# Optimization experiments

Hardware: AMD Instinct MI355X
Metric: run time of the kernel (lower is better)

Reference implementation:

```python
import jax, jax.numpy as jnp
import numpy as np

DIM = 2048
H = 16
D = 128          # head_dim
INNER = H * D    # == DIM
N_IMG = 257
EPS = 1e-6


def rms_norm(x, scale, eps=EPS):
    # flax nnx.RMSNorm over last axis: x * rsqrt(mean(x^2)+eps) * scale
    ms = jnp.mean(jnp.square(x), axis=-1, keepdims=True)
    return x * jax.lax.rsqrt(ms + eps) * scale


def sdpa(q, k, v):
    # q: (B,S,H,D), k/v: (B,L,H,D) -> (B,S,H,D); matches jax.nn.dot_product_attention
    scale = 1.0 / jnp.sqrt(jnp.asarray(D, q.dtype))
    scores = jnp.einsum('bshd,blhd->bhsl', q, k) * scale
    attn = jax.nn.softmax(scores, axis=-1)
    return jnp.einsum('bhsl,blhd->bshd', attn, v)


def setup_inputs() -> dict:
    key = jax.random.key(0)
    ks = jax.random.split(key, 16)
    std = 1.0 / np.sqrt(DIM)
    inp = {
        'x': jax.random.normal(ks[0], (2, 4096, DIM), jnp.float32),
        'context': jax.random.normal(ks[1], (2, 769, DIM), jnp.float32),
        'q_w': jax.random.normal(ks[2], (DIM, INNER), jnp.float32) * std,
        'q_b': jnp.zeros((INNER,), jnp.float32),
        'k_w': jax.random.normal(ks[3], (DIM, INNER), jnp.float32) * std,
        'k_b': jnp.zeros((INNER,), jnp.float32),
        'v_w': jax.random.normal(ks[4], (DIM, INNER), jnp.float32) * std,
        'v_b': jnp.zeros((INNER,), jnp.float32),
        'ki_w': jax.random.normal(ks[5], (DIM, INNER), jnp.float32) * std,
        'ki_b': jnp.zeros((INNER,), jnp.float32),
        'vi_w': jax.random.normal(ks[6], (DIM, INNER), jnp.float32) * std,
        'vi_b': jnp.zeros((INNER,), jnp.float32),
        'o_w': jax.random.normal(ks[7], (INNER, DIM), jnp.float32) * std,
        'o_b': jnp.zeros((DIM,), jnp.float32),
        'nq_s': jnp.ones((INNER,), jnp.float32),
        'nkt_s': jnp.ones((INNER,), jnp.float32),
        'nki_s': jnp.ones((INNER,), jnp.float32),
    }
    return inp


def reference(x, context, q_w, q_b, k_w, k_b, v_w, v_b, ki_w, ki_b, vi_w, vi_b,
              o_w, o_b, nq_s, nkt_s, nki_s):
    B, S, _ = x.shape
    img_ctx = context[:, :N_IMG]
    txt_ctx = context[:, N_IMG:]

    q = rms_norm(x @ q_w + q_b, nq_s).reshape(B, S, H, D)

    k_txt = rms_norm(txt_ctx @ k_w + k_b, nkt_s).reshape(B, -1, H, D)
    v_txt = (txt_ctx @ v_w + v_b).reshape(B, -1, H, D)
    out_txt = sdpa(q, k_txt, v_txt)

    k_img = rms_norm(img_ctx @ ki_w + ki_b, nki_s).reshape(B, -1, H, D)
    v_img = (img_ctx @ vi_w + vi_b).reshape(B, -1, H, D)
    out_img = sdpa(q, k_img, v_img)

    out = (out_txt + out_img).reshape(B, S, INNER)
    return out @ o_w + o_b
```

## Files before the change

kernel.cpp:

```cpp
#include <hip/hip_runtime.h>

typedef unsigned short u16;
typedef short s8v __attribute__((ext_vector_type(8)));
typedef float f32x4 __attribute__((ext_vector_type(4)));

#define MFMA16(a, b, c) __builtin_amdgcn_mfma_f32_16x16x32_bf16((a), (b), (c), 0, 0, 0)
#define GLDS16(gp, lp)                                                         \
  __builtin_amdgcn_global_load_lds(                                            \
      (const __attribute__((address_space(1))) void*)(gp),                     \
      (__attribute__((address_space(3))) void*)(lp), 16, 0, 0)

__device__ __forceinline__ float bf2f(u16 u) {
  unsigned int i = ((unsigned int)u) << 16;
  float f;
  __builtin_memcpy(&f, &i, 4);
  return f;
}
__device__ __forceinline__ u16 f2bf(float f) {
  unsigned int u;
  __builtin_memcpy(&u, &f, 4);
  unsigned int r = (u + 0x7FFFu + ((u >> 16) & 1u)) >> 16;
  return (u16)r;
}

__global__ __launch_bounds__(256) void cvt_f32_bf16(const float* __restrict__ s,
                                                    u16* __restrict__ d, long n) {
  long i = ((long)blockIdx.x * 256 + threadIdx.x) * 4;
  if (i + 3 < n) {
    float4 v = *(const float4*)(s + i);
    ushort4 o;
    o.x = f2bf(v.x); o.y = f2bf(v.y); o.z = f2bf(v.z); o.w = f2bf(v.w);
    *(ushort4*)(d + i) = o;
  }
}

struct TransposeBatch {
  const float* src[6];
  u16* dst[6];
};

__global__ __launch_bounds__(256) void transpose2048_batch(TransposeBatch p) {
  const float* __restrict__ W = p.src[blockIdx.z];
  u16* __restrict__ Wt = p.dst[blockIdx.z];
  __shared__ u16 t[64][65];
  int c0 = blockIdx.x * 64, r0 = blockIdx.y * 64;
  int x = threadIdx.x & 63, y = threadIdx.x >> 6;
  for (int yy = y; yy < 64; yy += 4)
    t[yy][x] = f2bf(W[(long)(r0 + yy) * 2048 + c0 + x]);
  __syncthreads();
  for (int yy = y; yy < 64; yy += 4)
    Wt[(long)(c0 + yy) * 2048 + r0 + x] = t[x][yy];
}

template <int OUTF, int DUAL>
__global__ __launch_bounds__(256, 2) void gemm_bias_bt(
    const u16* __restrict__ A, const u16* __restrict__ Bt,
    const float* __restrict__ bias, const float* __restrict__ bias2,
    void* __restrict__ Yv, void* __restrict__ Yv2, int M, int rpb, int bstride,
    int roff) {
  __shared__ u16 smA[128 * 32];
  __shared__ u16 smB[128 * 32];
  const int tid = threadIdx.x;
  const int wave = tid >> 6, lane = tid & 63;
  const int lo = lane & 15, qd = lane >> 4;
  const int m0 = blockIdx.x * 128, n0 = blockIdx.y * 128;
  const int wm = (wave & 1) * 64, wn = (wave >> 1) * 64;

  const u16* aG[2];
  const u16* bG[2];
  u16* aL[2];
  u16* bL[2];
#pragma unroll
  for (int r = 0; r < 2; ++r) {
    int c = (wave * 2 + r) * 64 + lane;
    int row = c >> 2, seg = c & 3;
    int gr = m0 + row;
    if (gr > M - 1) gr = M - 1;
    long grow = (long)(gr / rpb) * bstride + roff + (gr % rpb);
    aG[r] = A + grow * 2048 + seg * 8;
    bG[r] = Bt + (long)(n0 + row) * 2048 + seg * 8;
    aL[r] = smA + (wave * 2 + r) * 512;
    bL[r] = smB + (wave * 2 + r) * 512;
  }

  f32x4 acc[4][4] = {};
  for (int k0 = 0; k0 < 2048; k0 += 32) {
    GLDS16(aG[0] + k0, aL[0]);
    GLDS16(aG[1] + k0, aL[1]);
    GLDS16(bG[0] + k0, bL[0]);
    GLDS16(bG[1] + k0, bL[1]);
    __syncthreads();
    s8v af[4], bf[4];
#pragma unroll
    for (int i = 0; i < 4; i++)
      af[i] = *(const s8v*)(smA + (wm + i * 16 + lo) * 32 + qd * 8);
#pragma unroll
    for (int i = 0; i < 4; i++)
      bf[i] = *(const s8v*)(smB + (wn + i * 16 + lo) * 32 + qd * 8);
#pragma unroll
    for (int i = 0; i < 4; i++)
#pragma unroll
      for (int j = 0; j < 4; j++) acc[i][j] = MFMA16(af[i], bf[j], acc[i][j]);
    __syncthreads();
  }
#pragma unroll
  for (int j = 0; j < 4; j++) {
    int nf = n0 + wn + j * 16 + lo;
    const float* bp = bias;
    void* yp = Yv;
    int n = nf;
    if (DUAL && nf >= 2048) {
      bp = bias2;
      yp = Yv2;
      n = nf - 2048;
    }
    float bv = bp[n];
#pragma unroll
    for (int i = 0; i < 4; i++) {
      int mb = m0 + wm + i * 16 + qd * 4;
#pragma unroll
      for (int r = 0; r < 4; r++) {
        int m = mb + r;
        if (m < M) {
          float val = acc[i][j][r] + bv;
          if (OUTF)
            ((float*)yp)[(long)m * 2048 + n] = val;
          else
            ((u16*)yp)[(long)m * 2048 + n] = f2bf(val);
        }
      }
    }
  }
}

__global__ __launch_bounds__(256) void rmsnorm_rows(u16* __restrict__ X,
                                                    const float* __restrict__ sc) {
  long row = blockIdx.x;
  u16* xr = X + row * 2048;
  int tid = threadIdx.x;
  s8v v = *(const s8v*)(xr + tid * 8);
  float f[8], ss = 0.f;
#pragma unroll
  for (int j = 0; j < 8; j++) {
    f[j] = bf2f((u16)v[j]);
    ss += f[j] * f[j];
  }
  for (int o = 1; o < 64; o <<= 1) ss += __shfl_xor(ss, o);
  __shared__ float wsum[4];
  if ((tid & 63) == 0) wsum[tid >> 6] = ss;
  __syncthreads();
  float tot = wsum[0] + wsum[1] + wsum[2] + wsum[3];
  float rs = rsqrtf(tot * (1.f / 2048.f) + 1e-6f);
  float4 s0 = *(const float4*)(sc + tid * 8);
  float4 s1 = *(const float4*)(sc + tid * 8 + 4);
  float scv[8] = {s0.x, s0.y, s0.z, s0.w, s1.x, s1.y, s1.z, s1.w};
  s8v o8;
#pragma unroll
  for (int j = 0; j < 8; j++) o8[j] = (short)f2bf(f[j] * rs * scv[j]);
  *(s8v*)(xr + tid * 8) = o8;
}

__global__ __launch_bounds__(256) void repack_vt(const u16* __restrict__ V,
                                                 u16* __restrict__ VT, int L,
                                                 int Lpad) {
  int bh = blockIdx.z;
  int b = bh >> 4, h = bh & 15;
  int l0 = blockIdx.x * 64, d0 = blockIdx.y * 64;
  __shared__ u16 t[64][65];
  int x = threadIdx.x & 63, y = threadIdx.x >> 6;
  for (int yy = y; yy < 64; yy += 4) {
    int l = l0 + yy;
    u16 val = 0;
    if (l < L) val = V[((long)(b * L + l)) * 2048 + h * 128 + d0 + x];
    t[yy][x] = val;
  }
  __syncthreads();
  for (int yy = y; yy < 64; yy += 4) {
    int d = d0 + yy;
    int l = l0 + x;
    if (l < Lpad) VT[((long)bh * 128 + d) * Lpad + l] = t[x][yy];
  }
}

template <int LT, int LPT, int NTT, int LI, int LPI, int NTI>
__global__ __launch_bounds__(256, 2) void cross_attn_fused(
    const u16* __restrict__ Q, const u16* __restrict__ Kt,
    const u16* __restrict__ VTt, const u16* __restrict__ Ki,
    const u16* __restrict__ VTi, u16* __restrict__ O) {
  const int tid = threadIdx.x, wave = tid >> 6, lane = tid & 63;
  const int lo = lane & 15, qd = lane >> 4;
  const int id = blockIdx.x;
  const int xp = id & 7, xr = id >> 3;
  const int t = xr & 31;
  const int f = xp * 4 + (xr >> 5);
  const int h = f & 15, b = f >> 4;
  const int q0 = t * 128 + wave * 32;

  __shared__ u16 smem[38912];
  u16* lk = smem;
  u16* lv = smem + 8192;
  u16* pls = smem + 16384;
  u16* oTs = smem + 21504;

  const u16* Kbt = Kt + ((long)b * LT) * 2048 + h * 128;
  const u16* VTbt = VTt + ((long)(b * 16 + h)) * 128 * LPT;
  const u16* Kbi = Ki + ((long)b * LI) * 2048 + h * 128;
  const u16* VTbi = VTi + ((long)(b * 16 + h)) * 128 * LPI;

  auto stage = [&](int pb, int gt) {
    const u16* Kb;
    const u16* VTb;
    int kt, L, LPAD;
    if (gt < NTT) {
      Kb = Kbt; VTb = VTbt; kt = gt; L = LT; LPAD = LPT;
    } else {
      Kb = Kbi; VTb = VTbi; kt = gt - NTT; L = LI; LPAD = LPI;
    }
#pragma unroll
    for (int j = 0; j < 2; ++j) {
      int ci = (wave * 2 + j) * 64 + lane;
      int r = ci >> 4, c = ci & 15;
      int key = kt * 32 + r;
      if (key > L - 1) key = L - 1;
      const u16* src = Kb + (long)key * 2048 + (c ^ (r & 7)) * 8;
      GLDS16(src, &lk[pb * 4096 + (wave * 2 + j) * 512]);
    }
#pragma unroll
    for (int j = 0; j < 2; ++j) {
      int ci = (wave * 2 + j) * 64 + lane;
      int d = ci >> 2, c = ci & 3;
      const u16* src = VTb + (long)d * LPAD + kt * 32 + (c ^ ((d >> 1) & 3)) * 8;
      GLDS16(src, &lv[pb * 4096 + (wave * 2 + j) * 512]);
    }
  };

  s8v aq[2][4];
#pragma unroll
  for (int qf = 0; qf < 2; ++qf) {
    const u16* qp =
        Q + ((long)(b * 4096 + q0 + qf * 16 + lo)) * 2048 + h * 128 + qd * 8;
#pragma unroll
    for (int ds = 0; ds < 4; ++ds) aq[qf][ds] = *(const s8v*)(qp + ds * 32);
  }

  const float SC = 0.08838834764831845f;
  const int vsw = (lo >> 1) & 3;

  auto tile_step = [&](int pb, int ktile, int Lcur, f32x4 (&oacc)[2][8],
                       float (&lsum)[2][4]) {
    s8v bk[2][4];
#pragma unroll
    for (int nf = 0; nf < 2; ++nf) {
      int r = nf * 16 + lo;
#pragma unroll
      for (int ds = 0; ds < 4; ++ds) {
        int cp = (ds * 4 + qd) ^ (r & 7);
        bk[nf][ds] = *(const s8v*)(&lk[pb * 4096 + r * 128 + cp * 8]);
      }
    }
    f32x4 sacc[2][2] = {};
    __builtin_amdgcn_s_setprio(1);
#pragma unroll
    for (int qf = 0; qf < 2; ++qf)
#pragma unroll
      for (int nf = 0; nf < 2; ++nf)
#pragma unroll
        for (int ds = 0; ds < 4; ++ds)
          sacc[qf][nf] = MFMA16(aq[qf][ds], bk[nf][ds], sacc[qf][nf]);
    __builtin_amdgcn_s_setprio(0);
    u16* pw = pls + wave * 1280;
#pragma unroll
    for (int qf = 0; qf < 2; ++qf)
#pragma unroll
      for (int nf = 0; nf < 2; ++nf) {
        int key = ktile * 32 + nf * 16 + lo;
        bool msk = key >= Lcur;
#pragma unroll
        for (int r = 0; r < 4; ++r) {
          float s = fminf(fmaf(sacc[qf][nf][r], SC, -12.f), 50.f);
          float p = msk ? 0.f : __expf(s);
          lsum[qf][r] += p;
          pw[(qf * 16 + qd * 4 + r) * 40 + nf * 16 + lo] = f2bf(p);
        }
      }
    s8v pa[2];
#pragma unroll
    for (int qf = 0; qf < 2; ++qf)
      pa[qf] = *(const s8v*)(pw + (qf * 16 + lo) * 40 + qd * 8);
    __builtin_amdgcn_s_setprio(1);
#pragma unroll
    for (int df = 0; df < 8; ++df) {
      int d = df * 16 + lo;
      s8v bv = *(const s8v*)(&lv[pb * 4096 + d * 32 + (qd ^ vsw) * 8]);
      oacc[0][df] = MFMA16(pa[0], bv, oacc[0][df]);
      oacc[1][df] = MFMA16(pa[1], bv, oacc[1][df]);
    }
    __builtin_amdgcn_s_setprio(0);
  };

  stage(0, 0);
  __syncthreads();

  u16* ep = oTs + wave * 4352;

  {
    f32x4 oT[2][8] = {};
    float lsT[2][4] = {};
#pragma unroll 2
    for (int kt = 0; kt < NTT; ++kt) {
      const int pb = kt & 1;
      stage(pb ^ 1, kt + 1);
      tile_step(pb, kt, LT, oT, lsT);
      __syncthreads();
    }
#pragma unroll
    for (int qf = 0; qf < 2; ++qf)
#pragma unroll
      for (int r = 0; r < 4; ++r) {
        float a = lsT[qf][r];
        for (int o = 1; o < 16; o <<= 1) a += __shfl_xor(a, o);
        lsT[qf][r] = 1.f / a;
      }
#pragma unroll
    for (int qf = 0; qf < 2; ++qf)
#pragma unroll
      for (int df = 0; df < 8; ++df)
#pragma unroll
        for (int r = 0; r < 4; ++r)
          ep[(qf * 16 + qd * 4 + r) * 136 + df * 16 + lo] =
              f2bf(oT[qf][df][r] * lsT[qf][r]);
  }

  f32x4 oI[2][8] = {};
  float lsI[2][4] = {};
#pragma unroll 2
  for (int kt = 0; kt < NTI; ++kt) {
    const int pb = kt & 1;
    if (kt + 1 < NTI) stage(pb ^ 1, NTT + kt + 1);
    tile_step(pb, kt, LI, oI, lsI);
    if (kt + 1 < NTI) __syncthreads();
  }

#pragma unroll
  for (int qf = 0; qf < 2; ++qf)
#pragma unroll
    for (int r = 0; r < 4; ++r) {
      float c = lsI[qf][r];
      for (int o = 1; o < 16; o <<= 1) c += __shfl_xor(c, o);
      lsI[qf][r] = 1.f / c;
    }
#pragma unroll
  for (int qf = 0; qf < 2; ++qf)
#pragma unroll
    for (int df = 0; df < 8; ++df)
#pragma unroll
      for (int r = 0; r < 4; ++r) {
        int idx = (qf * 16 + qd * 4 + r) * 136 + df * 16 + lo;
        float val = bf2f(ep[idx]) + oI[qf][df][r] * lsI[qf][r];
        ep[idx] = f2bf(val);
      }
  const int row = lane >> 1, half = lane & 1;
  const u16* srcp = ep + row * 136 + half * 64;
  u16* gdst = O + ((long)(b * 4096 + q0 + row)) * 2048 + h * 128 + half * 64;
#pragma unroll
  for (int c = 0; c < 8; ++c) *(s8v*)(gdst + c * 8) = *(const s8v*)(srcp + c * 8);
}

extern "C" void kernel_launch(void* const* d_in, const int* in_sizes, int n_in,
                              void* d_out, int out_size, void* d_ws,
                              size_t ws_size, hipStream_t stream) {
  const float* x = (const float*)d_in[0];
  const float* ctx = (const float*)d_in[1];
  const float* q_w = (const float*)d_in[2];
  const float* q_b = (const float*)d_in[3];
  const float* k_w = (const float*)d_in[4];
  const float* k_b = (const float*)d_in[5];
  const float* v_w = (const float*)d_in[6];
  const float* v_b = (const float*)d_in[7];
  const float* ki_w = (const float*)d_in[8];
  const float* ki_b = (const float*)d_in[9];
  const float* vi_w = (const float*)d_in[10];
  const float* vi_b = (const float*)d_in[11];
  const float* o_w = (const float*)d_in[12];
  const float* o_b = (const float*)d_in[13];
  const float* nq_s = (const float*)d_in[14];
  const float* nkt_s = (const float*)d_in[15];
  const float* nki_s = (const float*)d_in[16];
  float* out = (float*)d_out;
  u16* ws = (u16*)d_ws;

  u16* w0 = ws;
  u16* w1 = ws + 4194304L;
  u16* q = ws + 8388608L;
  u16* attn = ws + 25165824L;
  u16* xb = attn;
  u16* vtxt = attn;
  u16* vimg = attn + 2097152L;
  u16* ktxt = ws + 41943040L;
  u16* kimg = ws + 44040192L;
  u16* vttxt = ws + 45092864L;
  u16* vtimg = ws + 47190016L;
  u16* ctxb = ws + 48369664L;

  dim3 tb(256);

  cvt_f32_bf16<<<3076, tb, 0, stream>>>(ctx, ctxb, 3149824L);
  TransposeBatch tp;
  tp.src[0] = q_w;  tp.dst[0] = w0;
  tp.src[1] = o_w;  tp.dst[1] = w1;
  tp.src[2] = k_w;  tp.dst[2] = q;
  tp.src[3] = v_w;  tp.dst[3] = q + 4194304L;
  tp.src[4] = ki_w; tp.dst[4] = q + 8388608L;
  tp.src[5] = vi_w; tp.dst[5] = q + 12582912L;
  transpose2048_batch<<<dim3(32, 32, 6), tb, 0, stream>>>(tp);

  gemm_bias_bt<0, 1><<<dim3(8, 32), tb, 0, stream>>>(
      ctxb, q, k_b, v_b, ktxt, vtxt, 1024, 512, 769, 257);
  gemm_bias_bt<0, 1><<<dim3(5, 32), tb, 0, stream>>>(
      ctxb, q + 8388608L, ki_b, vi_b, kimg, vimg, 514, 257, 769, 0);

  rmsnorm_rows<<<1024, tb, 0, stream>>>(ktxt, nkt_s);
  rmsnorm_rows<<<514, tb, 0, stream>>>(kimg, nki_s);
  repack_vt<<<dim3(8, 2, 32), tb, 0, stream>>>(vtxt, vttxt, 512, 512);
  repack_vt<<<dim3(5, 2, 32), tb, 0, stream>>>(vimg, vtimg, 257, 288);

  cvt_f32_bf16<<<16384, tb, 0, stream>>>(x, xb, 16777216L);
  gemm_bias_bt<0, 0><<<dim3(64, 16), tb, 0, stream>>>(
      xb, w0, q_b, nullptr, q, nullptr, 8192, 4096, 4096, 0);
  rmsnorm_rows<<<8192, tb, 0, stream>>>(q, nq_s);

  cross_attn_fused<512, 512, 16, 257, 288, 9><<<1024, tb, 0, stream>>>(
      q, ktxt, vttxt, kimg, vtimg, attn);

  gemm_bias_bt<1, 0><<<dim3(64, 16), tb, 0, stream>>>(
      attn, w1, o_b, nullptr, out, nullptr, 8192, 4096, 4096, 0);
}
```

Baseline: 626.4 us.

## Add 256x256-tile double-buffered GEMM for the Q and output projections

```diff
diff --git a/kernel.cpp b/kernel.cpp
--- a/kernel.cpp
+++ b/kernel.cpp
@@ -128,6 +128,103 @@
           else
             ((u16*)yp)[(long)m * 2048 + n] = f2bf(val);
         }
+      }
+    }
+  }
+}
+
+template <int OUTF>
+__global__ __launch_bounds__(512, 2) void gemm256(
+    const u16* __restrict__ A, const u16* __restrict__ Bt,
+    const float* __restrict__ bias, void* __restrict__ Yv) {
+  __shared__ u16 smA[2][16384];
+  __shared__ u16 smB[2][16384];
+  const int tid = threadIdx.x;
+  const int wave = tid >> 6, lane = tid & 63;
+  const int lo = lane & 15, qd = lane >> 4;
+  const int m0 = blockIdx.x * 256, n0 = blockIdx.y * 256;
+  const int wm = (wave >> 2) * 128, wn = (wave & 3) * 64;
+  const int wbase = (tid & ~63);
+
+  auto stage_h = [&](int b, int t, int half) {
+#pragma unroll
+    for (int j = half * 2; j < half * 2 + 2; ++j) {
+      int ci = j * 512 + tid;
+      int r = ci >> 3, c = ci & 7;
+      GLDS16(A + (long)(m0 + r) * 2048 + t * 64 + ((c ^ (r & 7)) << 3),
+             &smA[b][(j * 512 + wbase) * 8]);
+    }
+#pragma unroll
+    for (int j = half * 2; j < half * 2 + 2; ++j) {
+      int ci = j * 512 + tid;
+      int r = ci >> 3, c = ci & 7;
+      GLDS16(Bt + (long)(n0 + r) * 2048 + t * 64 + ((c ^ (r & 7)) << 3),
+             &smB[b][(j * 512 + wbase) * 8]);
+    }
+  };
+  auto rdA = [&](int b, int ks, int mf) {
+    int r = wm + mf * 16 + lo;
+    int sc = (ks * 4 + qd) ^ (r & 7);
+    return *(const s8v*)(&smA[b][r * 64 + sc * 8]);
+  };
+  auto rdB = [&](int b, int ks, int nf) {
+    int r = wn + nf * 16 + lo;
+    int sc = (ks * 4 + qd) ^ (r & 7);
+    return *(const s8v*)(&smB[b][r * 64 + sc * 8]);
+  };
+
+  f32x4 acc[8][4] = {};
+  stage_h(0, 0, 0); stage_h(0, 0, 1);
+  stage_h(1, 1, 0); stage_h(1, 1, 1);
+  asm volatile("s_waitcnt vmcnt(8)" ::: "memory");
+  __builtin_amdgcn_s_barrier();
+
+  for (int t = 0; t < 32; ++t) {
+    const int b = t & 1;
+    s8v af[8], bf[4];
+#pragma unroll
+    for (int mf = 0; mf < 8; ++mf) af[mf] = rdA(b, 0, mf);
+#pragma unroll
+    for (int nf = 0; nf < 4; ++nf) bf[nf] = rdB(b, 0, nf);
+    if (t < 31) stage_h(b ^ 1, t + 1, 0);
+    __builtin_amdgcn_s_setprio(1);
+#pragma unroll
+    for (int mf = 0; mf < 8; ++mf)
+#pragma unroll
+      for (int nf = 0; nf < 4; ++nf)
+        acc[mf][nf] = MFMA16(af[mf], bf[nf], acc[mf][nf]);
+    __builtin_amdgcn_s_setprio(0);
+    __builtin_amdgcn_s_barrier();
+#pragma unroll
+    for (int mf = 0; mf < 8; ++mf) af[mf] = rdA(b, 1, mf);
+#pragma unroll
+    for (int nf = 0; nf < 4; ++nf) bf[nf] = rdB(b, 1, nf);
+    if (t < 31) stage_h(b ^ 1, t + 1, 1);
+    __builtin_amdgcn_s_setprio(1);
+#pragma unroll
+    for (int mf = 0; mf < 8; ++mf)
+#pragma unroll
+      for (int nf = 0; nf < 4; ++nf)
+        acc[mf][nf] = MFMA16(af[mf], bf[nf], acc[mf][nf]);
+    __builtin_amdgcn_s_setprio(0);
+    asm volatile("s_waitcnt vmcnt(0)" ::: "memory");
+    __builtin_amdgcn_s_barrier();
+  }
+
+#pragma unroll
+  for (int nf = 0; nf < 4; ++nf) {
+    int n = n0 + wn + nf * 16 + lo;
+    float bv = bias[n];
+#pragma unroll
+    for (int mf = 0; mf < 8; ++mf) {
+      int mb = m0 + wm + mf * 16 + qd * 4;
+#pragma unroll
+      for (int r = 0; r < 4; ++r) {
+        float val = acc[mf][nf][r] + bv;
+        if (OUTF)
+          ((float*)Yv)[(long)(mb + r) * 2048 + n] = val;
+        else
+          ((u16*)Yv)[(long)(mb + r) * 2048 + n] = f2bf(val);
       }
     }
   }
@@ -425,13 +522,11 @@
   repack_vt<<<dim3(5, 2, 32), tb, 0, stream>>>(vimg, vtimg, 257, 288);
 
   cvt_f32_bf16<<<16384, tb, 0, stream>>>(x, xb, 16777216L);
-  gemm_bias_bt<0, 0><<<dim3(64, 16), tb, 0, stream>>>(
-      xb, w0, q_b, nullptr, q, nullptr, 8192, 4096, 4096, 0);
+  gemm256<0><<<dim3(32, 8), dim3(512), 0, stream>>>(xb, w0, q_b, q);
   rmsnorm_rows<<<8192, tb, 0, stream>>>(q, nq_s);
 
   cross_attn_fused<512, 512, 16, 257, 288, 9><<<1024, tb, 0, stream>>>(
       q, ktxt, vttxt, kimg, vtimg, attn);
 
-  gemm_bias_bt<1, 0><<<dim3(64, 16), tb, 0, stream>>>(
-      attn, w1, o_b, nullptr, out, nullptr, 8192, 4096, 4096, 0);
-}
+  gemm256<1><<<dim3(32, 8), dim3(512), 0, stream>>>(attn, w1, o_b, out);
+}
```

Result: faster. 575.5 us (-8.1%).
